# Performance work log

Hardware: AMD Instinct MI355X
Metric: run time of the kernel (lower is better)

## Reference

```python
import jax, jax.numpy as jnp
import numpy as np

D_MODEL = 1024
N_HEADS = 16
D_K = D_MODEL // N_HEADS


def setup_inputs() -> dict:
    key = jax.random.key(0)
    ks = jax.random.split(key, 11)
    B, L = 2, 2048
    s = 1.0 / np.sqrt(D_MODEL)
    inp = {
        "Q": jax.random.normal(ks[0], (B, L, D_MODEL), jnp.float32),
        "K": jax.random.normal(ks[1], (B, L, D_MODEL), jnp.float32),
        "V": jax.random.normal(ks[2], (B, L, D_MODEL), jnp.float32),
        "Wq": jax.random.normal(ks[3], (D_MODEL, D_MODEL), jnp.float32) * s,
        "bq": jnp.zeros((D_MODEL,), jnp.float32),
        "Wk": jax.random.normal(ks[4], (D_MODEL, D_MODEL), jnp.float32) * s,
        "bk": jnp.zeros((D_MODEL,), jnp.float32),
        "Wv": jax.random.normal(ks[5], (D_MODEL, D_MODEL), jnp.float32) * s,
        "bv": jnp.zeros((D_MODEL,), jnp.float32),
        "Wo": jax.random.normal(ks[6], (D_MODEL, D_MODEL), jnp.float32) * s,
        "bo": jnp.zeros((D_MODEL,), jnp.float32),
    }
    return inp


def reference(Q, K, V, Wq, bq, Wk, bk, Wv, bv, Wo, bo):
    B, Lq, D = Q.shape
    Lk = K.shape[1]
    H, dk = N_HEADS, D_K
    # projections -> [B, H, L, dk]
    q = (Q @ Wq + bq).reshape(B, Lq, H, dk).transpose(0, 2, 1, 3)
    k = (K @ Wk + bk).reshape(B, Lk, H, dk).transpose(0, 2, 1, 3)
    v = (V @ Wv + bv).reshape(B, Lk, H, dk).transpose(0, 2, 1, 3)
    scores = jnp.einsum("bhqd,bhkd->bhqk", q, k) / jnp.sqrt(jnp.float32(dk))
    attn = jax.nn.softmax(scores, axis=-1)  # dropout = identity (eval mode)
    ctx = jnp.einsum("bhqk,bhkd->bhqd", attn, v)
    ctx = ctx.transpose(0, 2, 1, 3).reshape(B, Lq, D)
    return ctx @ Wo + bo
```

## Files before the change

kernel.cpp:

```cpp
#include <hip/hip_runtime.h>


typedef _Float16 h16;
typedef _Float16 half8 __attribute__((ext_vector_type(8)));
typedef _Float16 half4 __attribute__((ext_vector_type(4)));
typedef __fp16 fp16x2 __attribute__((ext_vector_type(2)));
typedef float f32x4 __attribute__((ext_vector_type(4)));

#define D_MODEL 1024
#define N_HEADS 16
#define D_HEAD  64
#define SEQ_L   2048
#define QSCALE   0.18033688011f
#define P_PITCH  272

#define GLD16(gp, lp)                                                  \
  __builtin_amdgcn_global_load_lds(                                    \
      (const __attribute__((address_space(1))) void*)(gp),             \
      (__attribute__((address_space(3))) void*)(lp), 16, 0, 0)

struct XArgs { const float* src[3]; h16* dst[3]; };

__global__ __launch_bounds__(256) void convert_x(XArgs xa) {
  const float* src = xa.src[blockIdx.y];
  h16* dst = xa.dst[blockIdx.y];
  size_t i = ((size_t)blockIdx.x * 256 + threadIdx.x) * 8;
  float4 a = *reinterpret_cast<const float4*>(src + i);
  float4 b = *reinterpret_cast<const float4*>(src + i + 4);
  half8 o = {(h16)a.x, (h16)a.y, (h16)a.z, (h16)a.w,
             (h16)b.x, (h16)b.y, (h16)b.z, (h16)b.w};
  *reinterpret_cast<half8*>(dst + i) = o;
}

struct WArgs { const float* w[4]; h16* wt[4]; };

__global__ __launch_bounds__(256) void convert_wt(WArgs wa) {
  int z = blockIdx.z;
  const float* W = wa.w[z];
  h16* Wt = wa.wt[z];
  float scale = (z == 0) ? QSCALE : 1.0f;
  int k0 = blockIdx.x * 64, n0 = blockIdx.y * 64;
  __shared__ h16 T[64][65];
  int tid = threadIdx.x;
#pragma unroll
  for (int q = 0; q < 4; q++) {
    int fi = q * 256 + tid;
    int r = fi >> 4, c4 = (fi & 15) * 4;
    float4 v = *reinterpret_cast<const float4*>(W + (size_t)(k0 + r) * D_MODEL + n0 + c4);
    T[c4 + 0][r] = (h16)(v.x * scale);
    T[c4 + 1][r] = (h16)(v.y * scale);
    T[c4 + 2][r] = (h16)(v.z * scale);
    T[c4 + 3][r] = (h16)(v.w * scale);
  }
  __syncthreads();
#pragma unroll
  for (int q = 0; q < 2; q++) {
    int fi = q * 256 + tid;
    int r = fi >> 3, g = fi & 7;
    half8 o;
#pragma unroll
    for (int j = 0; j < 8; j++) o[j] = T[r][g * 8 + j];
    *reinterpret_cast<half8*>(Wt + (size_t)(n0 + r) * D_MODEL + k0 + g * 8) = o;
  }
}

__global__ __launch_bounds__(256) void convert_bq(const float* bq, float* bqs) {
  int i = blockIdx.x * 256 + threadIdx.x;
  if (i < D_MODEL) bqs[i] = bq[i] * QSCALE;
}

template <int BN>
__device__ __forceinline__ void gemm_body(const h16* __restrict__ A,
                                          const h16* __restrict__ Bt,
                                          const float* __restrict__ bias,
                                          h16* __restrict__ outh,
                                          float* __restrict__ outf,
                                          int mode) {
  constexpr int JT = BN / 32;
  __shared__ __align__(16) h16 As[128 * 64];
  __shared__ __align__(16) h16 Bs[BN * 64];
  const int tid = threadIdx.x;
  const int lane = tid & 63;
  const int w = tid >> 6;
  const int wm = w >> 1, wn = w & 1;
  const int cl = lane & 15, s = lane >> 4;
  const int m0 = blockIdx.x * 128;
  const int n0 = blockIdx.y * BN;
  const int sr = lane >> 3, sg = lane & 7;

  const f32x4 zero = {0.f, 0.f, 0.f, 0.f};
  f32x4 acc[4][JT];
#pragma unroll
  for (int i = 0; i < 4; i++)
#pragma unroll
    for (int j = 0; j < JT; j++) acc[i][j] = zero;

  const h16* aw = A + (size_t)(m0 + w * 32) * D_MODEL;
  const h16* bw = Bt + (size_t)(n0 + w * (BN / 4)) * D_MODEL;

  for (int k0 = 0; k0 < D_MODEL; k0 += 64) {
#pragma unroll
    for (int issue = 0; issue < 4; issue++)
      GLD16(aw + (size_t)(issue * 8 + sr) * D_MODEL + k0 + sg * 8,
            As + (w * 32 + issue * 8) * 64);
    if (BN == 128) {
#pragma unroll
      for (int issue = 0; issue < 4; issue++)
        GLD16(bw + (size_t)(issue * 8 + sr) * D_MODEL + k0 + sg * 8,
              Bs + (w * 32 + issue * 8) * 64);
    } else {
#pragma unroll
      for (int issue = 0; issue < 2; issue++)
        GLD16(bw + (size_t)(issue * 8 + sr) * D_MODEL + k0 + sg * 8,
              Bs + (w * 16 + issue * 8) * 64);
    }
    __syncthreads();
    half8 af[2][4], bf[2][JT];
#pragma unroll
    for (int kk = 0; kk < 2; kk++) {
#pragma unroll
      for (int i = 0; i < 4; i++)
        af[kk][i] = *reinterpret_cast<const half8*>(
            As + (wm * 64 + i * 16 + cl) * 64 + kk * 32 + s * 8);
#pragma unroll
      for (int j = 0; j < JT; j++)
        bf[kk][j] = *reinterpret_cast<const half8*>(
            Bs + (wn * (BN / 2) + j * 16 + cl) * 64 + kk * 32 + s * 8);
    }
    __builtin_amdgcn_s_setprio(1);
#pragma unroll
    for (int kk = 0; kk < 2; kk++)
#pragma unroll
      for (int i = 0; i < 4; i++)
#pragma unroll
        for (int j = 0; j < JT; j++)
          acc[i][j] = __builtin_amdgcn_mfma_f32_16x16x32_f16(af[kk][i], bf[kk][j], acc[i][j], 0, 0, 0);
    __builtin_amdgcn_s_setprio(0);
    __syncthreads();
  }

#pragma unroll
  for (int i = 0; i < 4; i++)
#pragma unroll
    for (int j = 0; j < JT; j++) {
      int c = n0 + wn * (BN / 2) + j * 16 + cl;
      float bv = bias[c];
      int mb = m0 + wm * 64 + i * 16 + s * 4;
      if (mode == 0) {
#pragma unroll
        for (int r = 0; r < 4; r++)
          outh[(size_t)(mb + r) * D_MODEL + c] = (h16)(acc[i][j][r] + bv);
      } else if (mode == 1) {
        int bb = mb >> 11;
        int h = c >> 6, d = c & 63;
        size_t rowbase = ((size_t)(bb * N_HEADS + h) * D_HEAD + d) * SEQ_L;
#pragma unroll
        for (int r = 0; r < 4; r++) {
          int kv = (mb + r) & 2047;
          int kvl = kv & 127;
          int pos = (((kvl & 15) << 3) | (kvl >> 4)) ^ ((d & 7) << 3);
          outh[rowbase + (kv & ~127) + pos] = (h16)(acc[i][j][r] + bv);
        }
      } else if (mode == 3) {
#pragma unroll
        for (int r = 0; r < 4; r++) {
          int m = mb + r;
          int bb = m >> 11, l = m & 2047;
          int h = c >> 6, d = c & 63;
          int dsw = (((d >> 3) ^ (l & 7)) << 3) | (d & 7);
          outh[((size_t)(bb * N_HEADS + h) * SEQ_L + l) * D_HEAD + dsw] =
              (h16)(acc[i][j][r] + bv);
        }
      } else {
#pragma unroll
        for (int r = 0; r < 4; r++)
          outf[(size_t)(mb + r) * D_MODEL + c] = acc[i][j][r] + bv;
      }
    }
}

struct ProjArgs {
  const h16* A[3];
  const h16* W[3];
  const float* b[3];
  h16* out[3];
};

__global__ __launch_bounds__(256, 3) void proj_kernel(ProjArgs pa) {
  int z = blockIdx.z;
  int mode = (z == 0) ? 0 : (z == 1) ? 3 : 1;
  gemm_body<128>(pa.A[z], pa.W[z], pa.b[z], pa.out[z], nullptr, mode);
}

__global__ __launch_bounds__(256, 2) void out_kernel(const h16* __restrict__ A,
                                                     const h16* __restrict__ Wt,
                                                     const float* __restrict__ b,
                                                     float* __restrict__ out) {
  gemm_body<64>(A, Wt, b, nullptr, out, 2);
}

__global__ __launch_bounds__(512, 2) void attn_kernel(const h16* __restrict__ Qh,
                                                      const h16* __restrict__ Kh,
                                                      const h16* __restrict__ Vt,
                                                      h16* __restrict__ ctx) {
  __shared__ __align__(16) char smem[102400];
  char* Ks = smem;
  char* Vs = smem + 16384;
  char* Ps = smem + 32768;
  const int tid = threadIdx.x;
  const int lane = tid & 63;
  const int w = tid >> 6;
  char* Pw = Ps + w * (32 * P_PITCH);
  int lid = blockIdx.x;
  int xcd = lid & 7, slot = lid >> 3;
  int bh = xcd * 4 + (slot & 3);
  int qt = slot >> 2;
  const int b = bh >> 4, h = bh & 15;
  const int q0 = qt * 256 + w * 32;
  const int cl = lane & 15, s = lane >> 4;

  const h16* Kb = Kh + (size_t)bh * SEQ_L * D_HEAD;
  const h16* Vb = Vt + (size_t)bh * D_HEAD * SEQ_L;

  half8 qf[2][2];
#pragma unroll
  for (int qr = 0; qr < 2; qr++)
#pragma unroll
    for (int kk = 0; kk < 2; kk++)
      qf[qr][kk] = *reinterpret_cast<const half8*>(
          Qh + (size_t)(b * SEQ_L + q0 + qr * 16 + cl) * D_MODEL + h * D_HEAD + kk * 32 + s * 8);

  const f32x4 zero = {0.f, 0.f, 0.f, 0.f};
  f32x4 acc[2][4];
#pragma unroll
  for (int qr = 0; qr < 2; qr++)
#pragma unroll
    for (int td = 0; td < 4; td++) acc[qr][td] = zero;
  float lrow[2][4];
#pragma unroll
  for (int qr = 0; qr < 2; qr++)
#pragma unroll
    for (int rg = 0; rg < 4; rg++) lrow[qr][rg] = 0.f;

  for (int kv0 = 0; kv0 < SEQ_L; kv0 += 128) {
#pragma unroll
    for (int issue = 0; issue < 2; issue++) {
      GLD16(Kb + (size_t)(kv0 + w * 16 + issue * 8) * D_HEAD + lane * 8,
            (h16*)Ks + (w * 16 + issue * 8) * D_HEAD);
    }
#pragma unroll
    for (int issue = 0; issue < 2; issue++) {
      GLD16(Vb + (size_t)(w * 8 + issue * 4 + (lane >> 4)) * SEQ_L + kv0 + (lane & 15) * 8,
            (h16*)Vs + (w * 8 + issue * 4) * 128);
    }
    __syncthreads();

    f32x4 sc[2][8];
#pragma unroll
    for (int t = 0; t < 8; t++) {
      int r = t * 16 + cl;
      half8 bf0 = *reinterpret_cast<const half8*>(Ks + r * 128 + ((s ^ (r & 7)) << 4));
      half8 bf1 = *reinterpret_cast<const half8*>(Ks + r * 128 + (((4 + s) ^ (r & 7)) << 4));
      __builtin_amdgcn_s_setprio(1);
      sc[0][t] = __builtin_amdgcn_mfma_f32_16x16x32_f16(qf[0][0], bf0, zero, 0, 0, 0);
      sc[0][t] = __builtin_amdgcn_mfma_f32_16x16x32_f16(qf[0][1], bf1, sc[0][t], 0, 0, 0);
      sc[1][t] = __builtin_amdgcn_mfma_f32_16x16x32_f16(qf[1][0], bf0, zero, 0, 0, 0);
      sc[1][t] = __builtin_amdgcn_mfma_f32_16x16x32_f16(qf[1][1], bf1, sc[1][t], 0, 0, 0);
      __builtin_amdgcn_s_setprio(0);
    }

#pragma unroll
    for (int qr = 0; qr < 2; qr++)
#pragma unroll
      for (int rg = 0; rg < 4; rg++) {
        float p[8];
        float rs = 0.f;
#pragma unroll
        for (int t = 0; t < 8; t++) {
          p[t] = exp2f(sc[qr][t][rg]);
          rs += p[t];
        }
        union { half8 v8; fp16x2 v2[4]; } u;
#pragma unroll
        for (int i = 0; i < 4; i++)
          u.v2[i] = __builtin_amdgcn_cvt_pkrtz(p[2 * i], p[2 * i + 1]);
        *reinterpret_cast<half8*>(
            Pw + (qr * 16 + s * 4 + rg) * P_PITCH + cl * 16) = u.v8;
        lrow[qr][rg] += rs;
      }

#pragma unroll
    for (int kvs = 0; kvs < 4; kvs++) {
      int g = kvs * 4 + s;
      half8 pf0 = *reinterpret_cast<const half8*>(Pw + cl * P_PITCH + g * 16);
      half8 pf1 = *reinterpret_cast<const half8*>(Pw + (16 + cl) * P_PITCH + g * 16);
#pragma unroll
      for (int td = 0; td < 4; td++) {
        int d = td * 16 + cl;
        half8 vf = *reinterpret_cast<const half8*>(Vs + d * 256 + ((g ^ (d & 7)) << 4));
        __builtin_amdgcn_s_setprio(1);
        acc[0][td] = __builtin_amdgcn_mfma_f32_16x16x32_f16(pf0, vf, acc[0][td], 0, 0, 0);
        acc[1][td] = __builtin_amdgcn_mfma_f32_16x16x32_f16(pf1, vf, acc[1][td], 0, 0, 0);
        __builtin_amdgcn_s_setprio(0);
      }
    }
    __syncthreads();
  }

#pragma unroll
  for (int qr = 0; qr < 2; qr++)
#pragma unroll
    for (int rg = 0; rg < 4; rg++) {
      float l = lrow[qr][rg];
#pragma unroll
      for (int msk = 1; msk < 16; msk <<= 1) l += __shfl_xor(l, msk);
      lrow[qr][rg] = l;
    }

#pragma unroll
  for (int qr = 0; qr < 2; qr++)
#pragma unroll
    for (int td = 0; td < 4; td++)
#pragma unroll
      for (int rg = 0; rg < 4; rg++) {
        int row = q0 + qr * 16 + s * 4 + rg;
        int d = td * 16 + cl;
        float v = acc[qr][td][rg] / lrow[qr][rg];
        ctx[(size_t)(b * SEQ_L + row) * D_MODEL + h * D_HEAD + d] = (h16)v;
      }
}

extern "C" void kernel_launch(void* const* d_in, const int* in_sizes, int n_in,
                              void* d_out, int out_size, void* d_ws, size_t ws_size,
                              hipStream_t stream) {
  const float* Q = (const float*)d_in[0];
  const float* K = (const float*)d_in[1];
  const float* V = (const float*)d_in[2];
  const float* Wq = (const float*)d_in[3];
  const float* bq = (const float*)d_in[4];
  const float* Wk = (const float*)d_in[5];
  const float* bk = (const float*)d_in[6];
  const float* Wv = (const float*)d_in[7];
  const float* bv = (const float*)d_in[8];
  const float* Wo = (const float*)d_in[9];
  const float* bo = (const float*)d_in[10];
  float* out = (float*)d_out;

  char* ws = (char*)d_ws;
  const size_t MB = 1024 * 1024;
  h16* Xh[3] = {(h16*)(ws), (h16*)(ws + 8 * MB), (h16*)(ws + 16 * MB)};
  h16* Wt[4] = {(h16*)(ws + 24 * MB), (h16*)(ws + 26 * MB),
                (h16*)(ws + 28 * MB), (h16*)(ws + 30 * MB)};
  h16* Qh = (h16*)(ws + 32 * MB);
  h16* Kh = (h16*)(ws + 40 * MB);
  h16* Vt = (h16*)(ws + 48 * MB);
  float* bqs = (float*)(ws + 56 * MB);
  h16* ctx = Xh[0];

  XArgs xa;
  xa.src[0] = Q; xa.src[1] = K; xa.src[2] = V;
  xa.dst[0] = Xh[0]; xa.dst[1] = Xh[1]; xa.dst[2] = Xh[2];
  convert_x<<<dim3(2048, 3), 256, 0, stream>>>(xa);

  WArgs wa;
  wa.w[0] = Wq; wa.w[1] = Wk; wa.w[2] = Wv; wa.w[3] = Wo;
  wa.wt[0] = Wt[0]; wa.wt[1] = Wt[1]; wa.wt[2] = Wt[2]; wa.wt[3] = Wt[3];
  convert_wt<<<dim3(16, 16, 4), 256, 0, stream>>>(wa);
  convert_bq<<<dim3(4), 256, 0, stream>>>(bq, bqs);

  ProjArgs pa;
  pa.A[0] = Xh[0]; pa.A[1] = Xh[1]; pa.A[2] = Xh[2];
  pa.W[0] = Wt[0]; pa.W[1] = Wt[1]; pa.W[2] = Wt[2];
  pa.b[0] = bqs;   pa.b[1] = bk;    pa.b[2] = bv;
  pa.out[0] = Qh;  pa.out[1] = Kh;  pa.out[2] = Vt;
  proj_kernel<<<dim3(32, 8, 3), 256, 0, stream>>>(pa);

  attn_kernel<<<dim3(256), 512, 0, stream>>>(Qh, Kh, Vt, ctx);

  out_kernel<<<dim3(32, 16), 256, 0, stream>>>(ctx, Wt[3], bo, out);
}
```

Before: 161.1 us.

## Double-buffer K/V tiles and keep P in registers via transposed score MFMA

The attention loop now double-buffers K and V tiles in LDS, issuing the next tile's global-to-LDS loads before computing the current one and waiting with partial vmcnt. Score MFMAs swap their operands so the result layout matches the A-operand layout of the PV MFMA, so P stays in registers and no longer round-trips through LDS. The V projection epilogue is changed to a permuted layout that allows half4 vector stores. The risks are the manual waitcnt and barrier sequencing and the reliance on the new V layout matching the fragment mapping.

```diff
diff --git a/kernel.cpp b/kernel.cpp
--- a/kernel.cpp
+++ b/kernel.cpp
@@ -12,7 +12,6 @@
 #define D_HEAD  64
 #define SEQ_L   2048
 #define QSCALE   0.18033688011f
-#define P_PITCH  272
 
 #define GLD16(gp, lp)                                                  \
   __builtin_amdgcn_global_load_lds(                                    \
@@ -152,23 +151,24 @@
           outh[(size_t)(mb + r) * D_MODEL + c] = (h16)(acc[i][j][r] + bv);
       } else if (mode == 1) {
         int bb = mb >> 11;
-        int h = c >> 6, d = c & 63;
-        size_t rowbase = ((size_t)(bb * N_HEADS + h) * D_HEAD + d) * SEQ_L;
-#pragma unroll
-        for (int r = 0; r < 4; r++) {
-          int kv = (mb + r) & 2047;
-          int kvl = kv & 127;
-          int pos = (((kvl & 15) << 3) | (kvl >> 4)) ^ ((d & 7) << 3);
-          outh[rowbase + (kv & ~127) + pos] = (h16)(acc[i][j][r] + bv);
-        }
+        int hh = c >> 6, d = c & 63;
+        size_t rowbase = ((size_t)(bb * N_HEADS + hh) * D_HEAD + d) * SEQ_L;
+        int kv = mb & 2047;
+        int kvl = kv & 127;
+        int G = ((kvl >> 5) << 2) | ((kvl >> 2) & 3);
+        int ht = (kvl >> 4) & 1;
+        int pos = ((G ^ (d & 7)) << 3) + ht * 4;
+        half4 o = {(h16)(acc[i][j][0] + bv), (h16)(acc[i][j][1] + bv),
+                   (h16)(acc[i][j][2] + bv), (h16)(acc[i][j][3] + bv)};
+        *reinterpret_cast<half4*>(outh + rowbase + (kv & ~127) + pos) = o;
       } else if (mode == 3) {
 #pragma unroll
         for (int r = 0; r < 4; r++) {
           int m = mb + r;
           int bb = m >> 11, l = m & 2047;
-          int h = c >> 6, d = c & 63;
+          int hh = c >> 6, d = c & 63;
           int dsw = (((d >> 3) ^ (l & 7)) << 3) | (d & 7);
-          outh[((size_t)(bb * N_HEADS + h) * SEQ_L + l) * D_HEAD + dsw] =
+          outh[((size_t)(bb * N_HEADS + hh) * SEQ_L + l) * D_HEAD + dsw] =
               (h16)(acc[i][j][r] + bv);
         }
       } else {
@@ -203,14 +203,10 @@
                                                       const h16* __restrict__ Kh,
                                                       const h16* __restrict__ Vt,
                                                       h16* __restrict__ ctx) {
-  __shared__ __align__(16) char smem[102400];
-  char* Ks = smem;
-  char* Vs = smem + 16384;
-  char* Ps = smem + 32768;
+  __shared__ __align__(16) char smem[65536];
   const int tid = threadIdx.x;
   const int lane = tid & 63;
   const int w = tid >> 6;
-  char* Pw = Ps + w * (32 * P_PITCH);
   int lid = blockIdx.x;
   int xcd = lid & 7, slot = lid >> 3;
   int bh = xcd * 4 + (slot & 3);
@@ -236,86 +232,97 @@
   for (int qr = 0; qr < 2; qr++)
 #pragma unroll
     for (int td = 0; td < 4; td++) acc[qr][td] = zero;
-  float lrow[2][4];
-#pragma unroll
-  for (int qr = 0; qr < 2; qr++)
-#pragma unroll
-    for (int rg = 0; rg < 4; rg++) lrow[qr][rg] = 0.f;
-
-  for (int kv0 = 0; kv0 < SEQ_L; kv0 += 128) {
-#pragma unroll
-    for (int issue = 0; issue < 2; issue++) {
-      GLD16(Kb + (size_t)(kv0 + w * 16 + issue * 8) * D_HEAD + lane * 8,
-            (h16*)Ks + (w * 16 + issue * 8) * D_HEAD);
-    }
-#pragma unroll
-    for (int issue = 0; issue < 2; issue++) {
-      GLD16(Vb + (size_t)(w * 8 + issue * 4 + (lane >> 4)) * SEQ_L + kv0 + (lane & 15) * 8,
-            (h16*)Vs + (w * 8 + issue * 4) * 128);
-    }
-    __syncthreads();
+  float lrp[2] = {0.f, 0.f};
+
+#define STAGE(buf, kv0)                                                        \
+  do {                                                                         \
+    char* Kd = smem + (buf) * 32768;                                           \
+    char* Vd = smem + (buf) * 32768 + 16384;                                   \
+    GLD16(Kb + (size_t)((kv0) + w * 16) * D_HEAD + lane * 8,                   \
+          (h16*)Kd + (w * 16) * D_HEAD);                                       \
+    GLD16(Kb + (size_t)((kv0) + w * 16 + 8) * D_HEAD + lane * 8,               \
+          (h16*)Kd + (w * 16 + 8) * D_HEAD);                                   \
+    GLD16(Vb + (size_t)(w * 8 + (lane >> 4)) * SEQ_L + (kv0) + (lane & 15) * 8,\
+          (h16*)Vd + (w * 8) * 128);                                           \
+    GLD16(Vb + (size_t)(w * 8 + 4 + (lane >> 4)) * SEQ_L + (kv0) + (lane & 15) * 8,\
+          (h16*)Vd + (w * 8 + 4) * 128);                                       \
+  } while (0)
+
+  STAGE(0, 0);
+  int cur = 0;
+  for (int t16 = 0; t16 < SEQ_L / 128; ++t16) {
+    if (t16 < SEQ_L / 128 - 1) {
+      STAGE(cur ^ 1, (t16 + 1) * 128);
+      asm volatile("s_waitcnt vmcnt(4)" ::: "memory");
+    } else {
+      asm volatile("s_waitcnt vmcnt(0)" ::: "memory");
+    }
+    __builtin_amdgcn_s_barrier();
+    char* Kc = smem + cur * 32768;
+    char* Vc = smem + cur * 32768 + 16384;
 
     f32x4 sc[2][8];
 #pragma unroll
     for (int t = 0; t < 8; t++) {
       int r = t * 16 + cl;
-      half8 bf0 = *reinterpret_cast<const half8*>(Ks + r * 128 + ((s ^ (r & 7)) << 4));
-      half8 bf1 = *reinterpret_cast<const half8*>(Ks + r * 128 + (((4 + s) ^ (r & 7)) << 4));
+      half8 bf0 = *reinterpret_cast<const half8*>(Kc + r * 128 + ((s ^ (r & 7)) << 4));
+      half8 bf1 = *reinterpret_cast<const half8*>(Kc + r * 128 + (((4 + s) ^ (r & 7)) << 4));
       __builtin_amdgcn_s_setprio(1);
-      sc[0][t] = __builtin_amdgcn_mfma_f32_16x16x32_f16(qf[0][0], bf0, zero, 0, 0, 0);
-      sc[0][t] = __builtin_amdgcn_mfma_f32_16x16x32_f16(qf[0][1], bf1, sc[0][t], 0, 0, 0);
-      sc[1][t] = __builtin_amdgcn_mfma_f32_16x16x32_f16(qf[1][0], bf0, zero, 0, 0, 0);
-      sc[1][t] = __builtin_amdgcn_mfma_f32_16x16x32_f16(qf[1][1], bf1, sc[1][t], 0, 0, 0);
+      sc[0][t] = __builtin_amdgcn_mfma_f32_16x16x32_f16(bf0, qf[0][0], zero, 0, 0, 0);
+      sc[0][t] = __builtin_amdgcn_mfma_f32_16x16x32_f16(bf1, qf[0][1], sc[0][t], 0, 0, 0);
+      sc[1][t] = __builtin_amdgcn_mfma_f32_16x16x32_f16(bf0, qf[1][0], zero, 0, 0, 0);
+      sc[1][t] = __builtin_amdgcn_mfma_f32_16x16x32_f16(bf1, qf[1][1], sc[1][t], 0, 0, 0);
       __builtin_amdgcn_s_setprio(0);
     }
 
-#pragma unroll
-    for (int qr = 0; qr < 2; qr++)
-#pragma unroll
-      for (int rg = 0; rg < 4; rg++) {
-        float p[8];
-        float rs = 0.f;
-#pragma unroll
-        for (int t = 0; t < 8; t++) {
-          p[t] = exp2f(sc[qr][t][rg]);
-          rs += p[t];
-        }
+    half8 paf[2][4];
+#pragma unroll
+    for (int qr = 0; qr < 2; qr++) {
+      float rs = 0.f;
+#pragma unroll
+      for (int kvs = 0; kvs < 4; kvs++) {
+        float p0 = exp2f(sc[qr][2 * kvs][0]), p1 = exp2f(sc[qr][2 * kvs][1]);
+        float p2 = exp2f(sc[qr][2 * kvs][2]), p3 = exp2f(sc[qr][2 * kvs][3]);
+        float p4 = exp2f(sc[qr][2 * kvs + 1][0]), p5 = exp2f(sc[qr][2 * kvs + 1][1]);
+        float p6 = exp2f(sc[qr][2 * kvs + 1][2]), p7 = exp2f(sc[qr][2 * kvs + 1][3]);
+        rs += (p0 + p1) + (p2 + p3) + (p4 + p5) + (p6 + p7);
         union { half8 v8; fp16x2 v2[4]; } u;
-#pragma unroll
-        for (int i = 0; i < 4; i++)
-          u.v2[i] = __builtin_amdgcn_cvt_pkrtz(p[2 * i], p[2 * i + 1]);
-        *reinterpret_cast<half8*>(
-            Pw + (qr * 16 + s * 4 + rg) * P_PITCH + cl * 16) = u.v8;
-        lrow[qr][rg] += rs;
+        u.v2[0] = __builtin_amdgcn_cvt_pkrtz(p0, p1);
+        u.v2[1] = __builtin_amdgcn_cvt_pkrtz(p2, p3);
+        u.v2[2] = __builtin_amdgcn_cvt_pkrtz(p4, p5);
+        u.v2[3] = __builtin_amdgcn_cvt_pkrtz(p6, p7);
+        paf[qr][kvs] = u.v8;
       }
+      lrp[qr] += rs;
+    }
 
 #pragma unroll
     for (int kvs = 0; kvs < 4; kvs++) {
-      int g = kvs * 4 + s;
-      half8 pf0 = *reinterpret_cast<const half8*>(Pw + cl * P_PITCH + g * 16);
-      half8 pf1 = *reinterpret_cast<const half8*>(Pw + (16 + cl) * P_PITCH + g * 16);
+      int G = kvs * 4 + s;
 #pragma unroll
       for (int td = 0; td < 4; td++) {
         int d = td * 16 + cl;
-        half8 vf = *reinterpret_cast<const half8*>(Vs + d * 256 + ((g ^ (d & 7)) << 4));
+        half8 vf = *reinterpret_cast<const half8*>(Vc + d * 256 + ((G ^ (d & 7)) << 4));
         __builtin_amdgcn_s_setprio(1);
-        acc[0][td] = __builtin_amdgcn_mfma_f32_16x16x32_f16(pf0, vf, acc[0][td], 0, 0, 0);
-        acc[1][td] = __builtin_amdgcn_mfma_f32_16x16x32_f16(pf1, vf, acc[1][td], 0, 0, 0);
+        acc[0][td] = __builtin_amdgcn_mfma_f32_16x16x32_f16(paf[0][kvs], vf, acc[0][td], 0, 0, 0);
+        acc[1][td] = __builtin_amdgcn_mfma_f32_16x16x32_f16(paf[1][kvs], vf, acc[1][td], 0, 0, 0);
         __builtin_amdgcn_s_setprio(0);
       }
     }
-    __syncthreads();
-  }
-
-#pragma unroll
-  for (int qr = 0; qr < 2; qr++)
-#pragma unroll
-    for (int rg = 0; rg < 4; rg++) {
-      float l = lrow[qr][rg];
-#pragma unroll
-      for (int msk = 1; msk < 16; msk <<= 1) l += __shfl_xor(l, msk);
-      lrow[qr][rg] = l;
-    }
+    __builtin_amdgcn_s_barrier();
+    cur ^= 1;
+  }
+#undef STAGE
+
+  float lq[2][4];
+#pragma unroll
+  for (int qr = 0; qr < 2; qr++) {
+    float l = lrp[qr];
+    l += __shfl_xor(l, 16);
+    l += __shfl_xor(l, 32);
+#pragma unroll
+    for (int rg = 0; rg < 4; rg++) lq[qr][rg] = __shfl(l, s * 4 + rg);
+  }
 
 #pragma unroll
   for (int qr = 0; qr < 2; qr++)
@@ -325,7 +332,7 @@
       for (int rg = 0; rg < 4; rg++) {
         int row = q0 + qr * 16 + s * 4 + rg;
         int d = td * 16 + cl;
-        float v = acc[qr][td][rg] / lrow[qr][rg];
+        float v = acc[qr][td][rg] / lq[qr][rg];
         ctx[(size_t)(b * SEQ_L + row) * D_MODEL + h * D_HEAD + d] = (h16)v;
       }
 }
```

Result: faster. 139.9 us (-13.2%).
